# Performance work log

Hardware: AMD Instinct MI355X
Metric: run time of the kernel (lower is better)

Reference implementation:

```python
import jax, jax.numpy as jnp
import numpy as np

T, B, E, H = 256, 8, 512, 32
EXP = 512            # number of expanded (periodic-image) keys
SMOOTH = 20.0        # smooth_factor


def setup_inputs() -> dict:
    key = jax.random.key(0)
    ks = jax.random.split(key, 12)
    s = 1.0 / np.sqrt(E)
    return {
        "query": jax.random.normal(ks[0], (T, B, E), dtype=jnp.float32),
        "outcell_index": jax.random.randint(ks[1], (B, EXP), 0, T),
        "expand_mask": jax.random.bernoulli(ks[2], 0.1, (B, EXP)),
        "key_padding_mask": jax.random.bernoulli(ks[3], 0.1, (B, T)),
        "local_attention_weight": jax.random.uniform(ks[4], (B, T, T + EXP), dtype=jnp.float32),
        "Wq": jax.random.normal(ks[5], (E, E), dtype=jnp.float32) * s,
        "bq": jnp.zeros((E,), dtype=jnp.float32),
        "Wk": jax.random.normal(ks[6], (E, E), dtype=jnp.float32) * s,   # k_bias=False
        "Wv": jax.random.normal(ks[7], (E, E), dtype=jnp.float32) * s,
        "bv": jnp.zeros((E,), dtype=jnp.float32),
        "Wo": jax.random.normal(ks[8], (E, E), dtype=jnp.float32) * s,
        "bo": jnp.zeros((E,), dtype=jnp.float32),
    }


def reference(query, outcell_index, expand_mask, key_padding_mask,
              local_attention_weight, Wq, bq, Wk, Wv, bv, Wo, bo):
    t, b, e = query.shape
    hd = e // H
    # QKV projections (torch Linear: y = x @ W.T + b)
    q = jnp.einsum('tbe,fe->tbf', query, Wq) + bq
    k = jnp.einsum('tbe,fe->tbf', query, Wk)          # no k bias
    v = jnp.einsum('tbe,fe->tbf', query, Wv) + bv
    # PBC gather-expand K/V along the time axis
    oc = outcell_index.T[:, :, None]                  # [EXP, B, 1]
    k = jnp.concatenate([k, jnp.take_along_axis(k, oc, axis=0)], axis=0)  # [S,B,E]
    v = jnp.concatenate([v, jnp.take_along_axis(v, oc, axis=0)], axis=0)
    s_len = k.shape[0]
    # [len, B, E] -> [B, H, len, hd]
    qh = q.reshape(t, b, H, hd).transpose(1, 2, 0, 3)
    kh = k.reshape(s_len, b, H, hd).transpose(1, 2, 0, 3)
    vh = v.reshape(s_len, b, H, hd).transpose(1, 2, 0, 3)
    # NOTE: forward() never applies self.scaling in this path (faithful)
    scores = jnp.einsum('bhtd,bhsd->bhts', qh, kh)    # [B,H,T,S]
    law = local_attention_weight[:, None]             # [B,1,T,S]
    scores = (scores + SMOOTH) * law - SMOOTH         # smooth softmax
    kpm = jnp.concatenate([key_padding_mask, expand_mask], axis=1)  # [B,S]
    scores = jnp.where(kpm[:, None, None, :], -jnp.inf, scores)
    probs = jax.nn.softmax(scores, axis=-1)
    probs = probs * law                               # post-softmax reweight
    attn = jnp.einsum('bhts,bhsd->bhtd', probs, vh)   # [B,H,T,hd]
    attn = attn.transpose(2, 0, 1, 3).reshape(t, b, e)
    return jnp.einsum('tbe,fe->tbf', attn, Wo) + bo
```

## Files before the change

### kernel.cpp

```cpp
#include <hip/hip_runtime.h>
#include <stdint.h>

#define T_ 256
#define B_ 8
#define E_ 512
#define H_ 32
#define HD_ 16
#define EXP_ 512
#define S_ 768
#define M_ 2048
#define SMOOTH_ 20.0f
#define KSTR 20
#define VSTR 776
#define VTH  392
#define LOG2E_ 1.44269504f
#define MB0_  (-100.988655f)

typedef __attribute__((ext_vector_type(8)))  short bf16x8;
typedef __attribute__((ext_vector_type(4)))  float f32x4;
typedef __attribute__((ext_vector_type(16))) float f32x16;
typedef __attribute__((ext_vector_type(2)))  unsigned int uint32x2;

__device__ __forceinline__ unsigned int cvtpk(float a, float b)
{
    unsigned int r;
    asm("v_cvt_pk_bf16_f32 %0, %1, %2" : "=v"(r) : "v"(a), "v"(b));
    return r;
}
__device__ __forceinline__ ushort bf1(float a)
{
    unsigned int u = __float_as_uint(a);
    u = u + 0x7FFFu + ((u >> 16) & 1u);
    return (ushort)(u >> 16);
}

union U16 { uint4 u; bf16x8 v; };
union U8x2 { uint2 p[2]; bf16x8 v; };

__device__ __forceinline__ bf16x8 ld20(const ushort* base, int row, int hi)
{
    U8x2 u;
    const ushort* p = &base[row * KSTR + hi * 8];
    u.p[0] = *(const uint2*)(p);
    u.p[1] = *(const uint2*)(p + 4);
    return u.v;
}

__global__ __launch_bounds__(1024, 4)
void qkv_proj(const float* __restrict__ X,
              const float* __restrict__ Wq, const float* __restrict__ Wk,
              const float* __restrict__ Wv,
              const float* __restrict__ bq, const float* __restrict__ bv,
              const int* __restrict__ oc,
              ushort* __restrict__ wsK, ushort* __restrict__ wsV,
              ushort* __restrict__ wsQ)
{
    __shared__ __align__(16) char raw[87552];
    ushort* Ks  = (ushort*)(raw);
    ushort* Vt  = (ushort*)(raw + 30720);
    ushort* Qi  = (ushort*)(raw + 55552);

    const int bh  = blockIdx.x;
    const int b   = bh & 7;
    const int h   = bh >> 3;
    const int tid = threadIdx.x;
    const int w   = tid >> 6;
    const int l   = tid & 63;

    const int r0 = tid >> 3;
    const int c8 = tid & 7;
    const float* Xc0 = &X[((size_t)r0 * 8 + b) * E_ + c8 * 8];
    const float* Xc1 = Xc0 + (size_t)128 * 8 * E_;

    const int wr = tid >> 3;
    const bool wload = (tid < 384);
    const float* Wsel = (wr < 16) ? Wq : (wr < 32 ? Wk : Wv);
    const float* Wr = &Wsel[((size_t)(h * 16 + (wr & 15))) * E_ + c8 * 8];

    f32x4 acc[3];
#pragma unroll
    for (int m = 0; m < 3; ++m) acc[m] = (f32x4){0.f, 0.f, 0.f, 0.f};

    float4 xa0, xa1, xb0, xb1, wp0, wp1;
    xa0 = *(const float4*)&Xc0[0]; xa1 = *(const float4*)&Xc0[4];
    xb0 = *(const float4*)&Xc1[0]; xb1 = *(const float4*)&Xc1[4];
    if (wload) { wp0 = *(const float4*)&Wr[0]; wp1 = *(const float4*)&Wr[4]; }

    const int ln = l & 15;
    const int lg = l >> 4;

    for (int it = 0; it < 8; ++it) {
        ushort* Ad = (ushort*)(raw + (it & 1) * 43776);
        ushort* Bd = Ad + 18432;
        *(uint4*)&Ad[r0 * 72 + c8 * 8] =
            make_uint4(cvtpk(xa0.x, xa0.y), cvtpk(xa0.z, xa0.w),
                       cvtpk(xa1.x, xa1.y), cvtpk(xa1.z, xa1.w));
        *(uint4*)&Ad[(r0 + 128) * 72 + c8 * 8] =
            make_uint4(cvtpk(xb0.x, xb0.y), cvtpk(xb0.z, xb0.w),
                       cvtpk(xb1.x, xb1.y), cvtpk(xb1.z, xb1.w));
        if (wload)
            *(uint4*)&Bd[wr * 72 + c8 * 8] =
                make_uint4(cvtpk(wp0.x, wp0.y), cvtpk(wp0.z, wp0.w),
                           cvtpk(wp1.x, wp1.y), cvtpk(wp1.z, wp1.w));
        __syncthreads();
        if (it < 7) {
            Xc0 += 64; Xc1 += 64;
            xa0 = *(const float4*)&Xc0[0]; xa1 = *(const float4*)&Xc0[4];
            xb0 = *(const float4*)&Xc1[0]; xb1 = *(const float4*)&Xc1[4];
            if (wload) { Wr += 64; wp0 = *(const float4*)&Wr[0]; wp1 = *(const float4*)&Wr[4]; }
        }
#pragma unroll
        for (int kb = 0; kb < 2; ++kb) {
            bf16x8 af = *(const bf16x8*)&Ad[(w * 16 + ln) * 72 + kb * 32 + lg * 8];
#pragma unroll
            for (int m = 0; m < 3; ++m) {
                bf16x8 bfm = *(const bf16x8*)&Bd[(m * 16 + ln) * 72 + kb * 32 + lg * 8];
                acc[m] = __builtin_amdgcn_mfma_f32_16x16x32_bf16(af, bfm, acc[m], 0, 0, 0);
            }
        }
    }

    __syncthreads();

    {
        const float bqv = bq[h * 16 + ln];
        const float bvv = bv[h * 16 + ln];
#pragma unroll
        for (int r = 0; r < 4; ++r) {
            const int t = w * 16 + lg * 4 + r;
            Qi[t * KSTR + ln] = bf1(acc[0][r] + bqv);
            Ks[t * KSTR + ln] = bf1(acc[1][r]);
            Vt[ln * VSTR + t] = bf1(acc[2][r] + bvv);
        }
    }
    __syncthreads();

    if (tid < 512) {
        const int j   = tid;
        const int src = oc[b * EXP_ + j];
        const ushort* sp = &Ks[src * KSTR];
        ushort* dp = &Ks[(T_ + j) * KSTR];
        uint2 k0 = *(const uint2*)(sp);
        uint2 k1 = *(const uint2*)(sp + 4);
        uint2 k2 = *(const uint2*)(sp + 8);
        uint2 k3 = *(const uint2*)(sp + 12);
        *(uint2*)(dp)      = k0;
        *(uint2*)(dp + 4)  = k1;
        *(uint2*)(dp + 8)  = k2;
        *(uint2*)(dp + 12) = k3;
    } else {
        const int j   = tid - 512;
        const int src = oc[b * EXP_ + j];
#pragma unroll
        for (int d = 0; d < 16; ++d)
            Vt[d * VSTR + T_ + j] = Vt[d * VSTR + src];
    }
    __syncthreads();

    if (tid < 768) {
        const ushort* sp = &Ks[tid * KSTR];
        uint2 a0 = *(const uint2*)(sp);
        uint2 a1 = *(const uint2*)(sp + 4);
        uint2 a2 = *(const uint2*)(sp + 8);
        uint2 a3 = *(const uint2*)(sp + 12);
        ushort* gp = &wsK[((size_t)bh * 768 + tid) * 16];
        *(uint4*)(gp)     = make_uint4(a0.x, a0.y, a1.x, a1.y);
        *(uint4*)(gp + 8) = make_uint4(a2.x, a2.y, a3.x, a3.y);
    } else {
        const int r = tid - 768;
        const ushort* sp = &Qi[r * KSTR];
        uint2 a0 = *(const uint2*)(sp);
        uint2 a1 = *(const uint2*)(sp + 4);
        uint2 a2 = *(const uint2*)(sp + 8);
        uint2 a3 = *(const uint2*)(sp + 12);
        ushort* gp = &wsQ[((size_t)bh * 256 + r) * 16];
        *(uint4*)(gp)     = make_uint4(a0.x, a0.y, a1.x, a1.y);
        *(uint4*)(gp + 8) = make_uint4(a2.x, a2.y, a3.x, a3.y);
    }
    {
        const int d = tid >> 6;
        const int c = tid & 63;
        const ushort* sp = &Vt[d * VSTR + c * 12];
        uint2 v0 = *(const uint2*)(sp);
        uint2 v1 = *(const uint2*)(sp + 4);
        uint2 v2 = *(const uint2*)(sp + 8);
        ushort* gp = &wsV[(size_t)bh * 16 * 768 + d * 768 + c * 12];
        *(uint2*)(gp)     = v0;
        *(uint2*)(gp + 4) = v1;
        *(uint2*)(gp + 8) = v2;
    }
}

__global__ __launch_bounds__(512, 4)
void attn_half(const float* __restrict__ LAW,
               const int* __restrict__ kpm, const int* __restrict__ em,
               const ushort* __restrict__ wsK, const ushort* __restrict__ wsV,
               const ushort* __restrict__ wsQ,
               float* __restrict__ wsO, float* __restrict__ wsZ)
{
    __shared__ __align__(16) char raw[39680];
    ushort* Qi  = (ushort*)(raw);
    ushort* Ksh = (ushort*)(raw + 10240);
    ushort* Vth = (ushort*)(raw + 25600);
    float*  msf = (float*) (raw + 38144);

    const int bid = blockIdx.x;
    const int bh  = bid >> 1;
    const int sh  = bid & 1;
    const int b   = bh & 7;
    const int h   = bh >> 3;
    const int tid = threadIdx.x;
    const int w   = tid >> 6;
    const int l   = tid & 63;

    {
        const ushort* QgB = &wsQ[(size_t)bh * 256 * 16];
        const int r  = tid >> 1;
        const int hf = tid & 1;
        uint4 q = *(const uint4*)&QgB[r * 16 + hf * 8];
        ushort* qp = &Qi[r * KSTR + hf * 8];
        *(uint2*)(qp)     = make_uint2(q.x, q.y);
        *(uint2*)(qp + 4) = make_uint2(q.z, q.w);
    }
    if (tid < 384) {
        const ushort* kp = &wsK[((size_t)bh * 768 + sh * 384 + tid) * 16];
        uint4 k0 = *(const uint4*)(kp);
        uint4 k1 = *(const uint4*)(kp + 8);
        ushort* dp = &Ksh[tid * KSTR];
        *(uint2*)(dp)      = make_uint2(k0.x, k0.y);
        *(uint2*)(dp + 4)  = make_uint2(k0.z, k0.w);
        *(uint2*)(dp + 8)  = make_uint2(k1.x, k1.y);
        *(uint2*)(dp + 12) = make_uint2(k1.z, k1.w);
        const int s = sh * 384 + tid;
        const int m = (s < T_) ? kpm[b * T_ + s] : em[b * EXP_ + (s - T_)];
        msf[tid] = m ? -1.0e5f : MB0_;
    }
    {
        const int d = tid >> 5;
        const int c = tid & 31;
        const ushort* vp = &wsV[(size_t)bh * 16 * 768 + d * 768 + sh * 384 + c * 12];
        uint2 v0 = *(const uint2*)(vp);
        uint2 v1 = *(const uint2*)(vp + 4);
        uint2 v2 = *(const uint2*)(vp + 8);
        ushort* dp = &Vth[d * VTH + c * 12];
        *(uint2*)(dp)     = v0;
        *(uint2*)(dp + 4) = v1;
        *(uint2*)(dp + 8) = v2;
    }
    __syncthreads();

    const int slane = l & 31;
    const int hi    = l >> 5;
    const int tq    = w;

    bf16x8 qf = ld20(Qi, tq * 32 + slane, hi);

    const f32x16 zero16 = {0.f,0.f,0.f,0.f,0.f,0.f,0.f,0.f,
                           0.f,0.f,0.f,0.f,0.f,0.f,0.f,0.f};
    f32x16 oacc = zero16;
    float zp0 = 0.f, zp1 = 0.f, zp2 = 0.f, zp3 = 0.f;

    const float* lawb = &LAW[((size_t)b * T_ + tq * 32 + slane) * S_ + 4 * hi];
    const int ig0 = sh * 12;

    bf16x8 kf = ld20(Ksh, slane, hi);
    float4 g0 = *(const float4*)&lawb[ig0 * 32];
    float4 g1 = *(const float4*)&lawb[ig0 * 32 + 8];
    float4 g2 = *(const float4*)&lawb[ig0 * 32 + 16];
    float4 g3 = *(const float4*)&lawb[ig0 * 32 + 24];

#pragma unroll 2
    for (int ii = 0; ii < 12; ++ii) {
        const int iin = (ii + 1 < 12) ? (ii + 1) : 0;

        bf16x8 vf0 = *(const bf16x8*)&Vth[(l & 15) * VTH + ii * 32 + hi * 8];
        bf16x8 vf1 = *(const bf16x8*)&Vth[(l & 15) * VTH + ii * 32 + 16 + hi * 8];
        const float4 m0 = *(const float4*)&msf[ii * 32 + 4 * hi];
        const float4 m1 = *(const float4*)&msf[ii * 32 + 8 + 4 * hi];
        const float4 m2 = *(const float4*)&msf[ii * 32 + 16 + 4 * hi];
        const float4 m3 = *(const float4*)&msf[ii * 32 + 24 + 4 * hi];

        f32x16 sc = __builtin_amdgcn_mfma_f32_32x32x16_bf16(kf, qf, zero16, 0, 0, 0);

        bf16x8 kfn = ld20(Ksh, iin * 32 + slane, hi);

        const float4 lwg[4] = {g0, g1, g2, g3};
        const float4 mbg[4] = {m0, m1, m2, m3};

#pragma unroll
        for (int ks = 0; ks < 2; ++ks) {
            float pp[8];
#pragma unroll
            for (int gi = 0; gi < 2; ++gi) {
                const int g = 2 * ks + gi;
                const float4 lw4 = lwg[g];
                const float4 mb4 = mbg[g];
                const float lwa[4] = {lw4.x, lw4.y, lw4.z, lw4.w};
                const float mba[4] = {mb4.x, mb4.y, mb4.z, mb4.w};
#pragma unroll
                for (int c = 0; c < 4; ++c) {
                    const float lwv = lwa[c];
                    const float lwK = lwv * LOG2E_;
                    const float arg = __builtin_fmaf(sc[8 * ks + 4 * gi + c], lwK,
                                      __builtin_fmaf(lwK, SMOOTH_, mba[c]));
                    const float e = __builtin_amdgcn_exp2f(arg);
                    if (c == 0) zp0 += e; else if (c == 1) zp1 += e;
                    else if (c == 2) zp2 += e; else zp3 += e;
                    pp[4 * gi + c] = e * lwv;
                }
            }
            const unsigned int cA0 = cvtpk(pp[0], pp[1]);
            const unsigned int cA2 = cvtpk(pp[2], pp[3]);
            const unsigned int cB0 = cvtpk(pp[4], pp[5]);
            const unsigned int cB2 = cvtpk(pp[6], pp[7]);
            uint32x2 s0 = __builtin_amdgcn_permlane32_swap(cA0, cB0, false, false);
            uint32x2 s1 = __builtin_amdgcn_permlane32_swap(cA2, cB2, false, false);
            U16 u;
            u.u = make_uint4(s0.x, s1.x, s0.y, s1.y);
            oacc = __builtin_amdgcn_mfma_f32_32x32x16_bf16(
                       u.v, ks ? vf1 : vf0, oacc, 0, 0, 0);
        }

        const int ign = ig0 + iin;
        g0 = *(const float4*)&lawb[ign * 32];
        g1 = *(const float4*)&lawb[ign * 32 + 8];
        g2 = *(const float4*)&lawb[ign * 32 + 16];
        g3 = *(const float4*)&lawb[ign * 32 + 24];
        kf = kfn;
    }

    float z = (zp0 + zp1) + (zp2 + zp3);
    z += __shfl_xor(z, 32);

    if ((l & 31) < 16) {
        const int dl = l & 15;
        float* Op = &wsO[(size_t)sh * M_ * E_ + (size_t)h * 16 + dl];
#pragma unroll
        for (int r = 0; r < 16; ++r) {
            const int t = tq * 32 + (r & 3) + 8 * (r >> 2) + 4 * hi;
            Op[(size_t)(t * 8 + b) * E_] = oacc[r];
        }
    }
    if (l < 32) {
        const int t = tq * 32 + l;
        wsZ[(size_t)sh * M_ * H_ + ((size_t)(t * 8 + b)) * H_ + h] = z;
    }
}

__global__ __launch_bounds__(256, 2)
void out_gemm(const float* __restrict__ wsO, const float* __restrict__ wsZ,
              const float* __restrict__ Wo, const float* __restrict__ bo,
              float* __restrict__ dst)
{
    __shared__ __align__(16) ushort sbuf[96 * 136];
    ushort* As = sbuf;
    ushort* Bs = sbuf + 32 * 136;

    const int n0 = blockIdx.x * 64;
    const int m0 = blockIdx.y * 32;

    const int tid = threadIdx.x;
    const int arow = tid >> 3;
    const int acol = (tid & 7) * 16;
    const int brow = tid >> 2;
    const int bcol = (tid & 3) * 32;

    const float* O0p = &wsO[(size_t)(m0 + arow) * E_ + acol];
    const float* O1p = O0p + (size_t)M_ * E_;
    const float* Zp  = &wsZ[(size_t)(m0 + arow) * H_];
    const float* Z1p = Zp + (size_t)M_ * H_;
    const float*  Wp = &Wo[(size_t)(n0 + brow) * E_ + bcol];

    f32x4 acc[2];
    acc[0] = (f32x4){0.f, 0.f, 0.f, 0.f};
    acc[1] = (f32x4){0.f, 0.f, 0.f, 0.f};

    float4 oa0 = *(const float4*)&O0p[0];
    float4 oa1 = *(const float4*)&O0p[4];
    float4 oa2 = *(const float4*)&O0p[8];
    float4 oa3 = *(const float4*)&O0p[12];
    float4 ob0 = *(const float4*)&O1p[0];
    float4 ob1 = *(const float4*)&O1p[4];
    float4 ob2 = *(const float4*)&O1p[8];
    float4 ob3 = *(const float4*)&O1p[12];
    float  zs  = Zp[acol >> 4] + Z1p[acol >> 4];
    float4 f0 = *(const float4*)&Wp[0];
    float4 f1 = *(const float4*)&Wp[4];
    float4 f2 = *(const float4*)&Wp[8];
    float4 f3 = *(const float4*)&Wp[12];
    float4 f4 = *(const float4*)&Wp[16];
    float4 f5 = *(const float4*)&Wp[20];
    float4 f6 = *(const float4*)&Wp[24];
    float4 f7 = *(const float4*)&Wp[28];

    const int l  = tid & 63;
    const int w  = tid >> 6;
    const int wm = w & 1;
    const int wn = w >> 1;
    const int lq = l >> 4;
    const int ln = l & 15;

    for (int it = 0; it < 4; ++it) {
        __syncthreads();
        {
            const float inv = (zs > 0.f) ? 1.f / zs : 0.f;
            const float c0 = (oa0.x + ob0.x) * inv, c1 = (oa0.y + ob0.y) * inv;
            const float c2 = (oa0.z + ob0.z) * inv, c3 = (oa0.w + ob0.w) * inv;
            const float c4 = (oa1.x + ob1.x) * inv, c5 = (oa1.y + ob1.y) * inv;
            const float c6 = (oa1.z + ob1.z) * inv, c7 = (oa1.w + ob1.w) * inv;
            const float c8 = (oa2.x + ob2.x) * inv, c9 = (oa2.y + ob2.y) * inv;
            const float ca = (oa2.z + ob2.z) * inv, cb = (oa2.w + ob2.w) * inv;
            const float cc = (oa3.x + ob3.x) * inv, cd = (oa3.y + ob3.y) * inv;
            const float ce = (oa3.z + ob3.z) * inv, cf = (oa3.w + ob3.w) * inv;
            *(uint4*)&As[arow * 136 + acol] =
                make_uint4(cvtpk(c0, c1), cvtpk(c2, c3), cvtpk(c4, c5), cvtpk(c6, c7));
            *(uint4*)&As[arow * 136 + acol + 8] =
                make_uint4(cvtpk(c8, c9), cvtpk(ca, cb), cvtpk(cc, cd), cvtpk(ce, cf));
        }
        *(uint4*)&Bs[brow * 136 + bcol]      = make_uint4(cvtpk(f0.x, f0.y), cvtpk(f0.z, f0.w),
                                                          cvtpk(f1.x, f1.y), cvtpk(f1.z, f1.w));
        *(uint4*)&Bs[brow * 136 + bcol + 8]  = make_uint4(cvtpk(f2.x, f2.y), cvtpk(f2.z, f2.w),
                                                          cvtpk(f3.x, f3.y), cvtpk(f3.z, f3.w));
        *(uint4*)&Bs[brow * 136 + bcol + 16] = make_uint4(cvtpk(f4.x, f4.y), cvtpk(f4.z, f4.w),
                                                          cvtpk(f5.x, f5.y), cvtpk(f5.z, f5.w));
        *(uint4*)&Bs[brow * 136 + bcol + 24] = make_uint4(cvtpk(f6.x, f6.y), cvtpk(f6.z, f6.w),
                                                          cvtpk(f7.x, f7.y), cvtpk(f7.z, f7.w));
        __syncthreads();
        if (it < 3) {
            O0p += 128; O1p += 128; Wp += 128;
            oa0 = *(const float4*)&O0p[0];
            oa1 = *(const float4*)&O0p[4];
            oa2 = *(const float4*)&O0p[8];
            oa3 = *(const float4*)&O0p[12];
            ob0 = *(const float4*)&O1p[0];
            ob1 = *(const float4*)&O1p[4];
            ob2 = *(const float4*)&O1p[8];
            ob3 = *(const float4*)&O1p[12];
            zs  = Zp[(it + 1) * 8 + (acol >> 4)] + Z1p[(it + 1) * 8 + (acol >> 4)];
            f0 = *(const float4*)&Wp[0];
            f1 = *(const float4*)&Wp[4];
            f2 = *(const float4*)&Wp[8];
            f3 = *(const float4*)&Wp[12];
            f4 = *(const float4*)&Wp[16];
            f5 = *(const float4*)&Wp[20];
            f6 = *(const float4*)&Wp[24];
            f7 = *(const float4*)&Wp[28];
        }
#pragma unroll
        for (int kb = 0; kb < 4; ++kb) {
            bf16x8 af  = *(const bf16x8*)&As[(wm * 16 + ln) * 136 + kb * 32 + lq * 8];
            bf16x8 bv0 = *(const bf16x8*)&Bs[(wn * 32 + ln) * 136 + kb * 32 + lq * 8];
            bf16x8 bv1 = *(const bf16x8*)&Bs[(wn * 32 + 16 + ln) * 136 + kb * 32 + lq * 8];
            acc[0] = __builtin_amdgcn_mfma_f32_16x16x32_bf16(af, bv0, acc[0], 0, 0, 0);
            acc[1] = __builtin_amdgcn_mfma_f32_16x16x32_bf16(af, bv1, acc[1], 0, 0, 0);
        }
    }

    const float bo0 = bo[n0 + wn * 32 + ln];
    const float bo1 = bo[n0 + wn * 32 + 16 + ln];

    __syncthreads();
    float* Lf = (float*)sbuf;
#pragma unroll
    for (int j = 0; j < 2; ++j) {
        const float bb = j ? bo1 : bo0;
        const f32x4 a = acc[j];
#pragma unroll
        for (int r = 0; r < 4; ++r)
            Lf[(wm * 16 + lq * 4 + r) * 68 + wn * 32 + j * 16 + ln] = a[r] + bb;
    }
    __syncthreads();

    {
        const int orow = tid >> 3;
        const int oc8  = (tid & 7) * 8;
        float* dp = &dst[(size_t)(m0 + orow) * E_ + n0 + oc8];
        float4 v0 = *(const float4*)&Lf[orow * 68 + oc8];
        float4 v1 = *(const float4*)&Lf[orow * 68 + oc8 + 4];
        *(float4*)&dp[0] = v0;
        *(float4*)&dp[4] = v1;
    }
}

extern "C" void kernel_launch(void* const* d_in, const int* in_sizes, int n_in,
                              void* d_out, int out_size, void* d_ws, size_t ws_size,
                              hipStream_t stream)
{
    const float* query = (const float*)d_in[0];
    const int*   oc    = (const int*)d_in[1];
    const int*   em    = (const int*)d_in[2];
    const int*   kpm   = (const int*)d_in[3];
    const float* law   = (const float*)d_in[4];
    const float* Wq    = (const float*)d_in[5];
    const float* bq    = (const float*)d_in[6];
    const float* Wk    = (const float*)d_in[7];
    const float* Wv    = (const float*)d_in[8];
    const float* bv    = (const float*)d_in[9];
    const float* Wo    = (const float*)d_in[10];
    const float* bo    = (const float*)d_in[11];
    float* out = (float*)d_out;

    char* ws = (char*)d_ws;
    ushort* wsK = (ushort*)(ws);
    ushort* wsV = (ushort*)(ws + 6291456);
    ushort* wsQ = (ushort*)(ws + 12582912);
    float*  wsO = (float*) (ws + 14680064);
    float*  wsZ = (float*) (ws + 23068672);

    qkv_proj<<<B_ * H_, 1024, 0, stream>>>(query, Wq, Wk, Wv, bq, bv, oc,
                                           wsK, wsV, wsQ);

    attn_half<<<B_ * H_ * 2, 512, 0, stream>>>(law, kpm, em, wsK, wsV, wsQ,
                                               wsO, wsZ);

    dim3 go(E_ / 64, M_ / 32, 1);
    out_gemm<<<go, 256, 0, stream>>>(wsO, wsZ, Wo, bo, out);
}
```

Measured before the change: 146.5 us.

## Replace per-head QKV projection with tiled GEMM and gather K/V in attention

The per-(batch,head) QKV projection kernel, which re-read the whole query slice for every head, is replaced by a standard 64x64-tiled bf16 MFMA GEMM over all 2048 rows and 1536 output columns, writing plain row-major Q/K/V. The periodic-image gather of K/V and the V transpose move into the attention kernel, which now indexes K/V rows through outcell_index when loading its tile. This cuts redundant X reads and gives far more blocks for parallelism, but the attention kernel now does scattered 32-byte row gathers and per-element transposed LDS stores for V. It also contains a redundant partial V load before the full uint4 load.

```diff
diff --git a/kernel.cpp b/kernel.cpp
--- a/kernel.cpp
+++ b/kernel.cpp
@@ -11,7 +11,6 @@
 #define M_ 2048
 #define SMOOTH_ 20.0f
 #define KSTR 20
-#define VSTR 776
 #define VTH  392
 #define LOG2E_ 1.44269504f
 #define MB0_  (-100.988655f)
@@ -26,12 +25,6 @@
     unsigned int r;
     asm("v_cvt_pk_bf16_f32 %0, %1, %2" : "=v"(r) : "v"(a), "v"(b));
     return r;
-}
-__device__ __forceinline__ ushort bf1(float a)
-{
-    unsigned int u = __float_as_uint(a);
-    u = u + 0x7FFFu + ((u >> 16) & 1u);
-    return (ushort)(u >> 16);
 }
 
 union U16 { uint4 u; bf16x8 v; };
@@ -46,156 +39,137 @@
     return u.v;
 }
 
-__global__ __launch_bounds__(1024, 4)
-void qkv_proj(const float* __restrict__ X,
+__global__ __launch_bounds__(256, 2)
+void qkv_gemm(const float* __restrict__ X,
               const float* __restrict__ Wq, const float* __restrict__ Wk,
               const float* __restrict__ Wv,
               const float* __restrict__ bq, const float* __restrict__ bv,
-              const int* __restrict__ oc,
-              ushort* __restrict__ wsK, ushort* __restrict__ wsV,
-              ushort* __restrict__ wsQ)
-{
-    __shared__ __align__(16) char raw[87552];
-    ushort* Ks  = (ushort*)(raw);
-    ushort* Vt  = (ushort*)(raw + 30720);
-    ushort* Qi  = (ushort*)(raw + 55552);
-
-    const int bh  = blockIdx.x;
-    const int b   = bh & 7;
-    const int h   = bh >> 3;
-    const int tid = threadIdx.x;
-    const int w   = tid >> 6;
-    const int l   = tid & 63;
-
-    const int r0 = tid >> 3;
-    const int c8 = tid & 7;
-    const float* Xc0 = &X[((size_t)r0 * 8 + b) * E_ + c8 * 8];
-    const float* Xc1 = Xc0 + (size_t)128 * 8 * E_;
-
-    const int wr = tid >> 3;
-    const bool wload = (tid < 384);
-    const float* Wsel = (wr < 16) ? Wq : (wr < 32 ? Wk : Wv);
-    const float* Wr = &Wsel[((size_t)(h * 16 + (wr & 15))) * E_ + c8 * 8];
-
-    f32x4 acc[3];
-#pragma unroll
-    for (int m = 0; m < 3; ++m) acc[m] = (f32x4){0.f, 0.f, 0.f, 0.f};
-
-    float4 xa0, xa1, xb0, xb1, wp0, wp1;
-    xa0 = *(const float4*)&Xc0[0]; xa1 = *(const float4*)&Xc0[4];
-    xb0 = *(const float4*)&Xc1[0]; xb1 = *(const float4*)&Xc1[4];
-    if (wload) { wp0 = *(const float4*)&Wr[0]; wp1 = *(const float4*)&Wr[4]; }
-
+              ushort* __restrict__ wsQb, ushort* __restrict__ wsKb,
+              ushort* __restrict__ wsVb)
+{
+    __shared__ __align__(16) ushort sbuf[2 * 64 * 72];
+    ushort* As = sbuf;
+    ushort* Bs = sbuf + 64 * 72;
+
+    const int n0 = blockIdx.x * 64;
+    const int m0 = blockIdx.y * 64;
+    const int which = n0 >> 9;
+    const int nn = n0 & 511;
+    const float* Wsel = (which == 0) ? Wq : (which == 1 ? Wk : Wv);
+    ushort* outb = (which == 0) ? wsQb : (which == 1 ? wsKb : wsVb);
+
+    const int tid  = threadIdx.x;
+    const int lrow = tid >> 2;
+    const int kq   = tid & 3;
+
+    const float* Xp = &X[(size_t)(m0 + lrow) * E_ + kq * 16];
+    const float* Wp = &Wsel[(size_t)(nn + lrow) * E_ + kq * 16];
+
+    f32x4 acc[2][2];
+#pragma unroll
+    for (int i = 0; i < 2; ++i)
+#pragma unroll
+        for (int j = 0; j < 2; ++j)
+            acc[i][j] = (f32x4){0.f, 0.f, 0.f, 0.f};
+
+    float4 a0 = *(const float4*)&Xp[0];
+    float4 a1 = *(const float4*)&Xp[4];
+    float4 a2 = *(const float4*)&Xp[8];
+    float4 a3 = *(const float4*)&Xp[12];
+    float4 f0 = *(const float4*)&Wp[0];
+    float4 f1 = *(const float4*)&Wp[4];
+    float4 f2 = *(const float4*)&Wp[8];
+    float4 f3 = *(const float4*)&Wp[12];
+
+    const int l  = tid & 63;
+    const int w  = tid >> 6;
+    const int wm = w & 1;
+    const int wn = w >> 1;
+    const int lq = l >> 4;
     const int ln = l & 15;
-    const int lg = l >> 4;
+
+    ushort* Aw = &As[lrow * 72 + kq * 16];
+    ushort* Bw = &Bs[lrow * 72 + kq * 16];
 
     for (int it = 0; it < 8; ++it) {
-        ushort* Ad = (ushort*)(raw + (it & 1) * 43776);
-        ushort* Bd = Ad + 18432;
-        *(uint4*)&Ad[r0 * 72 + c8 * 8] =
-            make_uint4(cvtpk(xa0.x, xa0.y), cvtpk(xa0.z, xa0.w),
-                       cvtpk(xa1.x, xa1.y), cvtpk(xa1.z, xa1.w));
-        *(uint4*)&Ad[(r0 + 128) * 72 + c8 * 8] =
-            make_uint4(cvtpk(xb0.x, xb0.y), cvtpk(xb0.z, xb0.w),
-                       cvtpk(xb1.x, xb1.y), cvtpk(xb1.z, xb1.w));
-        if (wload)
-            *(uint4*)&Bd[wr * 72 + c8 * 8] =
-                make_uint4(cvtpk(wp0.x, wp0.y), cvtpk(wp0.z, wp0.w),
-                           cvtpk(wp1.x, wp1.y), cvtpk(wp1.z, wp1.w));
+        __syncthreads();
+        *(uint4*)&Aw[0] = make_uint4(cvtpk(a0.x, a0.y), cvtpk(a0.z, a0.w),
+                                     cvtpk(a1.x, a1.y), cvtpk(a1.z, a1.w));
+        *(uint4*)&Aw[8] = make_uint4(cvtpk(a2.x, a2.y), cvtpk(a2.z, a2.w),
+                                     cvtpk(a3.x, a3.y), cvtpk(a3.z, a3.w));
+        *(uint4*)&Bw[0] = make_uint4(cvtpk(f0.x, f0.y), cvtpk(f0.z, f0.w),
+                                     cvtpk(f1.x, f1.y), cvtpk(f1.z, f1.w));
+        *(uint4*)&Bw[8] = make_uint4(cvtpk(f2.x, f2.y), cvtpk(f2.z, f2.w),
+                                     cvtpk(f3.x, f3.y), cvtpk(f3.z, f3.w));
         __syncthreads();
         if (it < 7) {
-            Xc0 += 64; Xc1 += 64;
-            xa0 = *(const float4*)&Xc0[0]; xa1 = *(const float4*)&Xc0[4];
-            xb0 = *(const float4*)&Xc1[0]; xb1 = *(const float4*)&Xc1[4];
-            if (wload) { Wr += 64; wp0 = *(const float4*)&Wr[0]; wp1 = *(const float4*)&Wr[4]; }
+            Xp += 64; Wp += 64;
+            a0 = *(const float4*)&Xp[0];
+            a1 = *(const float4*)&Xp[4];
+            a2 = *(const float4*)&Xp[8];
+            a3 = *(const float4*)&Xp[12];
+            f0 = *(const float4*)&Wp[0];
+            f1 = *(const float4*)&Wp[4];
+            f2 = *(const float4*)&Wp[8];
+            f3 = *(const float4*)&Wp[12];
         }
 #pragma unroll
         for (int kb = 0; kb < 2; ++kb) {
-            bf16x8 af = *(const bf16x8*)&Ad[(w * 16 + ln) * 72 + kb * 32 + lg * 8];
-#pragma unroll
-            for (int m = 0; m < 3; ++m) {
-                bf16x8 bfm = *(const bf16x8*)&Bd[(m * 16 + ln) * 72 + kb * 32 + lg * 8];
-                acc[m] = __builtin_amdgcn_mfma_f32_16x16x32_bf16(af, bfm, acc[m], 0, 0, 0);
-            }
-        }
+            bf16x8 af0 = *(const bf16x8*)&As[(32 * wm + ln) * 72 + 32 * kb + lq * 8];
+            bf16x8 af1 = *(const bf16x8*)&As[(32 * wm + 16 + ln) * 72 + 32 * kb + lq * 8];
+            bf16x8 bf0 = *(const bf16x8*)&Bs[(32 * wn + ln) * 72 + 32 * kb + lq * 8];
+            bf16x8 bf1 = *(const bf16x8*)&Bs[(32 * wn + 16 + ln) * 72 + 32 * kb + lq * 8];
+            acc[0][0] = __builtin_amdgcn_mfma_f32_16x16x32_bf16(af0, bf0, acc[0][0], 0, 0, 0);
+            acc[0][1] = __builtin_amdgcn_mfma_f32_16x16x32_bf16(af0, bf1, acc[0][1], 0, 0, 0);
+            acc[1][0] = __builtin_amdgcn_mfma_f32_16x16x32_bf16(af1, bf0, acc[1][0], 0, 0, 0);
+            acc[1][1] = __builtin_amdgcn_mfma_f32_16x16x32_bf16(af1, bf1, acc[1][1], 0, 0, 0);
+        }
+    }
+
+    float bo0 = 0.f, bo1 = 0.f;
+    if (which == 0) {
+        bo0 = bq[nn + 32 * wn + ln];
+        bo1 = bq[nn + 32 * wn + 16 + ln];
+    } else if (which == 2) {
+        bo0 = bv[nn + 32 * wn + ln];
+        bo1 = bv[nn + 32 * wn + 16 + ln];
     }
 
     __syncthreads();
+    float* Lf = (float*)sbuf;
+#pragma unroll
+    for (int j = 0; j < 2; ++j) {
+        const float bb = j ? bo1 : bo0;
+#pragma unroll
+        for (int i = 0; i < 2; ++i)
+#pragma unroll
+            for (int r = 0; r < 4; ++r)
+                Lf[(32 * wm + 16 * i + lq * 4 + r) * 68 + 32 * wn + 16 * j + ln] =
+                    acc[i][j][r] + bb;
+    }
+    __syncthreads();
 
     {
-        const float bqv = bq[h * 16 + ln];
-        const float bvv = bv[h * 16 + ln];
-#pragma unroll
-        for (int r = 0; r < 4; ++r) {
-            const int t = w * 16 + lg * 4 + r;
-            Qi[t * KSTR + ln] = bf1(acc[0][r] + bqv);
-            Ks[t * KSTR + ln] = bf1(acc[1][r]);
-            Vt[ln * VSTR + t] = bf1(acc[2][r] + bvv);
-        }
-    }
-    __syncthreads();
-
-    if (tid < 512) {
-        const int j   = tid;
-        const int src = oc[b * EXP_ + j];
-        const ushort* sp = &Ks[src * KSTR];
-        ushort* dp = &Ks[(T_ + j) * KSTR];
-        uint2 k0 = *(const uint2*)(sp);
-        uint2 k1 = *(const uint2*)(sp + 4);
-        uint2 k2 = *(const uint2*)(sp + 8);
-        uint2 k3 = *(const uint2*)(sp + 12);
-        *(uint2*)(dp)      = k0;
-        *(uint2*)(dp + 4)  = k1;
-        *(uint2*)(dp + 8)  = k2;
-        *(uint2*)(dp + 12) = k3;
-    } else {
-        const int j   = tid - 512;
-        const int src = oc[b * EXP_ + j];
-#pragma unroll
-        for (int d = 0; d < 16; ++d)
-            Vt[d * VSTR + T_ + j] = Vt[d * VSTR + src];
-    }
-    __syncthreads();
-
-    if (tid < 768) {
-        const ushort* sp = &Ks[tid * KSTR];
-        uint2 a0 = *(const uint2*)(sp);
-        uint2 a1 = *(const uint2*)(sp + 4);
-        uint2 a2 = *(const uint2*)(sp + 8);
-        uint2 a3 = *(const uint2*)(sp + 12);
-        ushort* gp = &wsK[((size_t)bh * 768 + tid) * 16];
-        *(uint4*)(gp)     = make_uint4(a0.x, a0.y, a1.x, a1.y);
-        *(uint4*)(gp + 8) = make_uint4(a2.x, a2.y, a3.x, a3.y);
-    } else {
-        const int r = tid - 768;
-        const ushort* sp = &Qi[r * KSTR];
-        uint2 a0 = *(const uint2*)(sp);
-        uint2 a1 = *(const uint2*)(sp + 4);
-        uint2 a2 = *(const uint2*)(sp + 8);
-        uint2 a3 = *(const uint2*)(sp + 12);
-        ushort* gp = &wsQ[((size_t)bh * 256 + r) * 16];
-        *(uint4*)(gp)     = make_uint4(a0.x, a0.y, a1.x, a1.y);
-        *(uint4*)(gp + 8) = make_uint4(a2.x, a2.y, a3.x, a3.y);
-    }
-    {
-        const int d = tid >> 6;
-        const int c = tid & 63;
-        const ushort* sp = &Vt[d * VSTR + c * 12];
-        uint2 v0 = *(const uint2*)(sp);
-        uint2 v1 = *(const uint2*)(sp + 4);
-        uint2 v2 = *(const uint2*)(sp + 8);
-        ushort* gp = &wsV[(size_t)bh * 16 * 768 + d * 768 + c * 12];
-        *(uint2*)(gp)     = v0;
-        *(uint2*)(gp + 4) = v1;
-        *(uint2*)(gp + 8) = v2;
+        const int orow = tid >> 3;
+        const int oc8  = (tid & 7) * 8;
+#pragma unroll
+        for (int hh = 0; hh < 2; ++hh) {
+            const int rr = orow + hh * 32;
+            float4 v0 = *(const float4*)&Lf[rr * 68 + oc8];
+            float4 v1 = *(const float4*)&Lf[rr * 68 + oc8 + 4];
+            *(uint4*)&outb[(size_t)(m0 + rr) * E_ + nn + oc8] =
+                make_uint4(cvtpk(v0.x, v0.y), cvtpk(v0.z, v0.w),
+                           cvtpk(v1.x, v1.y), cvtpk(v1.z, v1.w));
+        }
     }
 }
 
 __global__ __launch_bounds__(512, 4)
 void attn_half(const float* __restrict__ LAW,
                const int* __restrict__ kpm, const int* __restrict__ em,
-               const ushort* __restrict__ wsK, const ushort* __restrict__ wsV,
-               const ushort* __restrict__ wsQ,
+               const int* __restrict__ oc,
+               const ushort* __restrict__ wsQb, const ushort* __restrict__ wsKb,
+               const ushort* __restrict__ wsVb,
                float* __restrict__ wsO, float* __restrict__ wsZ)
 {
     __shared__ __align__(16) char raw[39680];
@@ -214,38 +188,37 @@
     const int l   = tid & 63;
 
     {
-        const ushort* QgB = &wsQ[(size_t)bh * 256 * 16];
         const int r  = tid >> 1;
         const int hf = tid & 1;
-        uint4 q = *(const uint4*)&QgB[r * 16 + hf * 8];
+        uint4 q = *(const uint4*)&wsQb[(size_t)(r * 8 + b) * E_ + h * 16 + hf * 8];
         ushort* qp = &Qi[r * KSTR + hf * 8];
         *(uint2*)(qp)     = make_uint2(q.x, q.y);
         *(uint2*)(qp + 4) = make_uint2(q.z, q.w);
     }
     if (tid < 384) {
-        const ushort* kp = &wsK[((size_t)bh * 768 + sh * 384 + tid) * 16];
-        uint4 k0 = *(const uint4*)(kp);
-        uint4 k1 = *(const uint4*)(kp + 8);
+        const int sg    = sh * 384 + tid;
+        const int tsrc  = (sg < T_) ? sg : oc[b * EXP_ + (sg - T_)];
+        const size_t mr = (size_t)(tsrc * 8 + b) * E_ + h * 16;
+        uint4 k0 = *(const uint4*)&wsKb[mr];
+        uint4 k1 = *(const uint4*)&wsKb[mr + 8];
         ushort* dp = &Ksh[tid * KSTR];
         *(uint2*)(dp)      = make_uint2(k0.x, k0.y);
         *(uint2*)(dp + 4)  = make_uint2(k0.z, k0.w);
         *(uint2*)(dp + 8)  = make_uint2(k1.x, k1.y);
         *(uint2*)(dp + 12) = make_uint2(k1.z, k1.w);
-        const int s = sh * 384 + tid;
-        const int m = (s < T_) ? kpm[b * T_ + s] : em[b * EXP_ + (s - T_)];
+        U16 vv;
+        vv.u.x = *((const uint*)&wsVb[mr]);
+        vv.u.y = *((const uint*)&wsVb[mr + 2]);
+        vv.u = *(const uint4*)&wsVb[mr];
+        uint4 v1 = *(const uint4*)&wsVb[mr + 8];
+        const ushort* ve0 = (const ushort*)&vv.u;
+        const ushort* ve1 = (const ushort*)&v1;
+#pragma unroll
+        for (int d = 0; d < 8; ++d) Vth[d * VTH + tid] = ve0[d];
+#pragma unroll
+        for (int d = 0; d < 8; ++d) Vth[(d + 8) * VTH + tid] = ve1[d];
+        const int m = (sg < T_) ? kpm[b * T_ + sg] : em[b * EXP_ + (sg - T_)];
         msf[tid] = m ? -1.0e5f : MB0_;
-    }
-    {
-        const int d = tid >> 5;
-        const int c = tid & 31;
-        const ushort* vp = &wsV[(size_t)bh * 16 * 768 + d * 768 + sh * 384 + c * 12];
-        uint2 v0 = *(const uint2*)(vp);
-        uint2 v1 = *(const uint2*)(vp + 4);
-        uint2 v2 = *(const uint2*)(vp + 8);
-        ushort* dp = &Vth[d * VTH + c * 12];
-        *(uint2*)(dp)     = v0;
-        *(uint2*)(dp + 4) = v1;
-        *(uint2*)(dp + 8) = v2;
     }
     __syncthreads();
 
@@ -501,17 +474,18 @@
     float* out = (float*)d_out;
 
     char* ws = (char*)d_ws;
-    ushort* wsK = (ushort*)(ws);
-    ushort* wsV = (ushort*)(ws + 6291456);
-    ushort* wsQ = (ushort*)(ws + 12582912);
-    float*  wsO = (float*) (ws + 14680064);
-    float*  wsZ = (float*) (ws + 23068672);
-
-    qkv_proj<<<B_ * H_, 1024, 0, stream>>>(query, Wq, Wk, Wv, bq, bv, oc,
-                                           wsK, wsV, wsQ);
-
-    attn_half<<<B_ * H_ * 2, 512, 0, stream>>>(law, kpm, em, wsK, wsV, wsQ,
-                                               wsO, wsZ);
+    ushort* wsQb = (ushort*)(ws);
+    ushort* wsKb = (ushort*)(ws + 2097152);
+    ushort* wsVb = (ushort*)(ws + 4194304);
+    float*  wsO  = (float*) (ws + 6291456);
+    float*  wsZ  = (float*) (ws + 14680064);
+
+    dim3 gq(1536 / 64, M_ / 64, 1);
+    qkv_gemm<<<gq, 256, 0, stream>>>(query, Wq, Wk, Wv, bq, bv,
+                                     wsQb, wsKb, wsVb);
+
+    attn_half<<<B_ * H_ * 2, 512, 0, stream>>>(law, kpm, em, oc,
+                                               wsQb, wsKb, wsVb, wsO, wsZ);
 
     dim3 go(E_ / 64, M_ / 32, 1);
     out_gemm<<<go, 256, 0, stream>>>(wsO, wsZ, Wo, bo, out);
```

New measurement: 144.1 us. Within noise of the previous version (-1.6%).
